# Kernel optimization log

Hardware: AMD Instinct MI355X
Metric: run time of the kernel (lower is better)

Reference implementation:

```python
import jax, jax.numpy as jnp
import numpy as np

H = 1024; NH = 16; HD = H // NH  # hidden, heads, head_dim

def setup_inputs() -> dict:
    key = jax.random.key(0)
    ks = jax.random.split(key, 9)
    s = 1.0 / np.sqrt(H)
    return {
        "hidden_states": jax.random.normal(ks[0], (2, 2048, H), jnp.float32),
        "Wq": jax.random.uniform(ks[1], (H, H), jnp.float32, -s, s),
        "bq": jnp.zeros((H,), jnp.float32),
        "Wk": jax.random.uniform(ks[2], (H, H), jnp.float32, -s, s),
        "bk": jnp.zeros((H,), jnp.float32),
        "Wv": jax.random.uniform(ks[3], (H, H), jnp.float32, -s, s),
        "bv": jnp.zeros((H,), jnp.float32),
        "Wo": jax.random.uniform(ks[4], (H, H), jnp.float32, -s, s),
        "bo": jnp.zeros((H,), jnp.float32),
    }

def reference(hidden_states, Wq, bq, Wk, bk, Wv, bv, Wo, bo):
    B, S, _ = hidden_states.shape
    def heads(x):  # [B,S,H] -> [B,NH,S,HD]
        return x.reshape(B, S, NH, HD).transpose(0, 2, 1, 3)
    q = heads(hidden_states @ Wq + bq)
    k = heads(hidden_states @ Wk + bk)
    v = heads(hidden_states @ Wv + bv)
    scores = jnp.einsum('bhqd,bhkd->bhqk', q, k) / jnp.sqrt(jnp.float32(HD))
    causal = jnp.where(jnp.tril(jnp.ones((S, S), bool)), 0.0, -jnp.inf)
    probs = jax.nn.softmax(scores + causal[None, None], axis=-1)
    ctx = jnp.einsum('bhqk,bhkd->bhqd', probs, v)
    ctx = ctx.transpose(0, 2, 1, 3).reshape(B, S, H)
    return ctx @ Wo + bo
```

## Files before the change

kernel.cpp:

```cpp
#include <hip/hip_runtime.h>
#include <hip/hip_bf16.h>

#define BB 2
#define SS 2048
#define HH 1024
#define NHH 16
#define HDD 64
#define MM (BB*SS)
#define QKV_N (3*HH)

typedef _Float16 f16x8 __attribute__((ext_vector_type(8)));
typedef _Float16 f16x4 __attribute__((ext_vector_type(4)));
typedef float f32x4 __attribute__((ext_vector_type(4)));

#define MFMA16(a,b,c)  __builtin_amdgcn_mfma_f32_16x16x32_f16((a),(b),(c),0,0,0)
#define MFMA16K16(a,b,c) __builtin_amdgcn_mfma_f32_16x16x16f16((a),(b),(c),0,0,0)

__device__ __forceinline__ void gl2lds16(const _Float16* g, _Float16* l) {
    __builtin_amdgcn_global_load_lds(
        (const __attribute__((address_space(1))) void*)g,
        (__attribute__((address_space(3))) void*)l, 16, 0, 0);
}

__device__ __forceinline__ float fexp2(float x) { return __builtin_amdgcn_exp2f(x); }

__global__ __launch_bounds__(256) void prep_kernel(
    const float* __restrict__ X,
    const float* __restrict__ W0, const float* __restrict__ W1,
    const float* __restrict__ W2, const float* __restrict__ W3,
    _Float16* __restrict__ Xh,
    _Float16* __restrict__ WqkvT, _Float16* __restrict__ WoT)
{
    __shared__ float t[64][65];
    int z = blockIdx.z;
    int tid = threadIdx.x;
    if (z == 4) {
        int base = (blockIdx.y * 16 + blockIdx.x) * 256 + tid;
        const float4* xin = (const float4*)X;
        f16x4* xout = (f16x4*)Xh;
#pragma unroll
        for (int i = 0; i < 16; ++i) {
            float4 v = xin[base + i * 65536];
            f16x4 hh = {(_Float16)v.x, (_Float16)v.y, (_Float16)v.z, (_Float16)v.w};
            xout[base + i * 65536] = hh;
        }
        return;
    }
    const float* src = (z == 0) ? W0 : (z == 1) ? W1 : (z == 2) ? W2 : W3;
    _Float16* dst = (z < 3) ? (WqkvT + (size_t)z * HH * HH) : WoT;
    int k0 = blockIdx.y * 64, n0 = blockIdx.x * 64;
#pragma unroll
    for (int p = 0; p < 4; ++p) {
        int row = p * 16 + (tid >> 4);
        int col4 = (tid & 15) * 4;
        float4 v = *(const float4*)&src[(size_t)(k0 + row) * HH + n0 + col4];
        t[row][col4 + 0] = v.x; t[row][col4 + 1] = v.y;
        t[row][col4 + 2] = v.z; t[row][col4 + 3] = v.w;
    }
    __syncthreads();
#pragma unroll
    for (int p = 0; p < 2; ++p) {
        int nc = p * 32 + (tid >> 3);
        int ch = tid & 7;
        f16x8 o;
#pragma unroll
        for (int j = 0; j < 8; ++j) o[j] = (_Float16)t[ch * 8 + j][nc];
        *(f16x8*)&dst[(size_t)(n0 + nc) * HH + k0 + ch * 8] = o;
    }
}

__global__ __launch_bounds__(256, 5) void gemm_qkv_kernel(
    const _Float16* __restrict__ A, const _Float16* __restrict__ Bt,
    const float* __restrict__ bias0, const float* __restrict__ bias1, const float* __restrict__ bias2,
    _Float16* __restrict__ Qh, _Float16* __restrict__ Kh, _Float16* __restrict__ Vt)
{
    const int K = HH;
    const int NT = K / 32;
    __shared__ _Float16 smem[16384];

    int row0 = blockIdx.y * 128, n0 = blockIdx.x * 128;
    int tid = threadIdx.x;
    int w = tid >> 6, l = tid & 63, m16 = l & 15, quad = l >> 4;
    int wm = w >> 1, wn = w & 1;

    int srow = w * 32 + (l >> 2);
    int sch = (l & 3) ^ ((l >> 2) & 3) ^ ((l >> 4) & 3);
    const _Float16* aptr = A + (size_t)(row0 + srow) * K + sch * 8;
    const _Float16* bptr = Bt + (size_t)(n0 + srow) * K + sch * 8;

    int gsw = (m16 & 3) ^ ((m16 >> 2) & 3);
    int acol = (quad ^ gsw) * 8;

    f32x4 zero4 = {0.f, 0.f, 0.f, 0.f};
    f32x4 acc[4][4];
#pragma unroll
    for (int i = 0; i < 4; ++i)
#pragma unroll
        for (int j = 0; j < 4; ++j) acc[i][j] = zero4;

    auto stage = [&](int t) {
        int s = (t & 1) * 4096;
        int k0 = t * 32;
        int ao = s + (w * 32) * 32;
        int bo = 8192 + s + (w * 32) * 32;
        gl2lds16(aptr + k0, smem + ao);
        gl2lds16(aptr + (size_t)16 * K + k0, smem + ao + 16 * 32);
        gl2lds16(bptr + k0, smem + bo);
        gl2lds16(bptr + (size_t)16 * K + k0, smem + bo + 16 * 32);
    };

    stage(0);
    for (int t = 0; t < NT; ++t) {
        asm volatile("s_barrier" ::: "memory");
        if (t + 1 < NT) {
            stage(t + 1);
            asm volatile("s_waitcnt vmcnt(4)" ::: "memory");
        } else {
            asm volatile("s_waitcnt vmcnt(0)" ::: "memory");
        }
        asm volatile("s_barrier" ::: "memory");

        const _Float16* Asr = smem + (t & 1) * 4096;
        const _Float16* Bsr = smem + 8192 + (t & 1) * 4096;
        f16x8 af[4], bf[4];
#pragma unroll
        for (int i = 0; i < 4; ++i)
            af[i] = *(const f16x8*)&Asr[(wm * 64 + i * 16 + m16) * 32 + acol];
#pragma unroll
        for (int j = 0; j < 4; ++j)
            bf[j] = *(const f16x8*)&Bsr[(wn * 64 + j * 16 + m16) * 32 + acol];
#pragma unroll
        for (int i = 0; i < 4; ++i)
#pragma unroll
            for (int j = 0; j < 4; ++j)
                acc[i][j] = MFMA16(af[i], bf[j], acc[i][j]);
    }

    int which = n0 >> 10;
    const float* bias = (which == 0) ? bias0 : (which == 1) ? bias1 : bias2;
    int b = row0 >> 11, s0 = row0 & 2047;

#pragma unroll
    for (int rh = 0; rh < 2; ++rh) {
        __syncthreads();
        if (wm == rh) {
#pragma unroll
            for (int j = 0; j < 4; ++j) {
                int n_local = wn * 64 + j * 16 + m16;
                float bi = bias[(n0 + n_local) & 1023];
#pragma unroll
                for (int i = 0; i < 4; ++i)
#pragma unroll
                    for (int r = 0; r < 4; ++r) {
                        int m_loc = i * 16 + quad * 4 + r;
                        float v = acc[i][j][r] + bi;
                        if (which == 0) v *= 0.18033688011112042f;
                        if (which == 2) smem[n_local * 68 + m_loc] = (_Float16)v;
                        else            smem[m_loc * 132 + n_local] = (_Float16)v;
                    }
            }
        }
        __syncthreads();
        int hs0 = s0 + rh * 64;
        if (which == 2) {
#pragma unroll
            for (int p = 0; p < 4; ++p) {
                int n_local = p * 32 + (tid >> 3);
                int schunk = tid & 7;
                f16x8 v = *(const f16x8*)&smem[n_local * 68 + schunk * 8];
                int nw = (n0 + n_local) & 1023;
                int hh = nw >> 6, d = nw & 63;
                *(f16x8*)&Vt[((size_t)(b * NHH + hh) * HDD + d) * SS + hs0 + schunk * 8] = v;
            }
        } else {
            _Float16* dst = (which == 0) ? Qh : Kh;
            int hh0 = (n0 & 1023) >> 6;
#pragma unroll
            for (int p = 0; p < 4; ++p) {
                int m_local = p * 16 + (tid >> 4);
                int seg = tid & 15;
                f16x8 v = *(const f16x8*)&smem[m_local * 132 + seg * 8];
                int hh = hh0 + (seg >> 3), d = (seg & 7) * 8;
                *(f16x8*)&dst[((size_t)(b * NHH + hh) * SS + hs0 + m_local) * HDD + d] = v;
            }
        }
    }
}

__global__ __launch_bounds__(256) void gemm_out_kernel(
    const _Float16* __restrict__ A, const _Float16* __restrict__ Bt,
    const float* __restrict__ bias0, float* __restrict__ Out)
{
    const int K = HH;
    const int NT = K / 32;
    __shared__ _Float16 smem[24576];

    int row0 = blockIdx.y * 128, n0 = blockIdx.x * 128;
    int tid = threadIdx.x;
    int w = tid >> 6, l = tid & 63, m16 = l & 15, quad = l >> 4;
    int wm = w >> 1, wn = w & 1;

    int srow = w * 32 + (l >> 2);
    int sch = (l & 3) ^ ((l >> 2) & 3) ^ ((l >> 4) & 3);
    const _Float16* aptr = A + (size_t)(row0 + srow) * K + sch * 8;
    const _Float16* bptr = Bt + (size_t)(n0 + srow) * K + sch * 8;

    int gsw = (m16 & 3) ^ ((m16 >> 2) & 3);
    int acol = (quad ^ gsw) * 8;

    f32x4 zero4 = {0.f, 0.f, 0.f, 0.f};
    f32x4 acc[4][4];
#pragma unroll
    for (int i = 0; i < 4; ++i)
#pragma unroll
        for (int j = 0; j < 4; ++j) acc[i][j] = zero4;

    auto stage = [&](int t, int s) {
        int k0 = t * 32;
        int ao = s * 4096 + (w * 32) * 32;
        int bo = 12288 + s * 4096 + (w * 32) * 32;
        gl2lds16(aptr + k0, smem + ao);
        gl2lds16(aptr + (size_t)16 * K + k0, smem + ao + 16 * 32);
        gl2lds16(bptr + k0, smem + bo);
        gl2lds16(bptr + (size_t)16 * K + k0, smem + bo + 16 * 32);
    };

    stage(0, 0);
    stage(1, 1);
    int cur = 0;
    for (int t = 0; t < NT; ++t) {
        if (t < NT - 1) asm volatile("s_waitcnt vmcnt(4)" ::: "memory");
        else            asm volatile("s_waitcnt vmcnt(0)" ::: "memory");
        asm volatile("s_barrier" ::: "memory");
        if (t + 2 < NT) {
            int nxt = cur + 2; if (nxt >= 3) nxt -= 3;
            stage(t + 2, nxt);
        }
        const _Float16* Asr = smem + cur * 4096;
        const _Float16* Bsr = smem + 12288 + cur * 4096;
        f16x8 af[4], bf[4];
#pragma unroll
        for (int i = 0; i < 4; ++i)
            af[i] = *(const f16x8*)&Asr[(wm * 64 + i * 16 + m16) * 32 + acol];
#pragma unroll
        for (int j = 0; j < 4; ++j)
            bf[j] = *(const f16x8*)&Bsr[(wn * 64 + j * 16 + m16) * 32 + acol];
#pragma unroll
        for (int i = 0; i < 4; ++i)
#pragma unroll
            for (int j = 0; j < 4; ++j)
                acc[i][j] = MFMA16(af[i], bf[j], acc[i][j]);
        cur = (cur == 2) ? 0 : cur + 1;
    }

#pragma unroll
    for (int j = 0; j < 4; ++j) {
        int n = n0 + wn * 64 + j * 16 + m16;
        float bi = bias0[n];
#pragma unroll
        for (int i = 0; i < 4; ++i)
#pragma unroll
            for (int r = 0; r < 4; ++r) {
                int mg = row0 + wm * 64 + i * 16 + quad * 4 + r;
                Out[(size_t)mg * HH + n] = acc[i][j][r] + bi;
            }
    }
}

__global__ __launch_bounds__(512, 4) void attn_kernel(
    const _Float16* __restrict__ Qh, const _Float16* __restrict__ Kh,
    const _Float16* __restrict__ Vt, _Float16* __restrict__ Ctx)
{
    __shared__ _Float16 KV[3 * 8192];

    int tid = threadIdx.x;
    int w = tid >> 6, l = tid & 63;
    int m16 = l & 15, quad = l >> 4;
    int b = blockIdx.z, h = blockIdx.y;
    int tA = blockIdx.x, tB = 31 - tA;
    int half = w >> 2, wq = w & 3;
    int myT = half ? tB : tA;

    const _Float16* Q = Qh + (size_t)(b * NHH + h) * SS * HDD;
    const _Float16* K = Kh + (size_t)(b * NHH + h) * SS * HDD;
    const _Float16* V = Vt + (size_t)(b * NHH + h) * HDD * SS;

    int q = myT * 64 + wq * 16 + m16;
    f16x8 aq0 = *(const f16x8*)(Q + (size_t)q * HDD + quad * 8);
    f16x8 aq1 = *(const f16x8*)(Q + (size_t)q * HDD + 32 + quad * 8);

    int srow = w * 8 + (l >> 3);
    int sch = (l & 7) ^ (l >> 3);
    const _Float16* kg = K + (size_t)srow * HDD + sch * 8;
    const _Float16* vg = V + (size_t)srow * SS + sch * 8;

    auto stage = [&](int t, int s) {
        int kt = t * 64;
        _Float16* kb = &KV[s * 8192];
        _Float16* vb = &KV[s * 8192 + 4096];
        gl2lds16(kg + (size_t)kt * HDD, kb + (w * 8) * 64);
        gl2lds16(vg + kt, vb + (w * 8) * 64);
    };

    int swz = m16 & 7;
    int cka = (quad ^ swz) * 8;
    int ckb = ((quad + 4) ^ swz) * 8;
    int vco[4];
#pragma unroll
    for (int s = 0; s < 4; ++s)
        vco[s] = (((s * 2 + (quad >> 1)) ^ swz) * 8) + (quad & 1) * 4;

    f32x4 zero4 = {0.f, 0.f, 0.f, 0.f};
    const f16x4 ones4 = {(_Float16)1.f, (_Float16)1.f, (_Float16)1.f, (_Float16)1.f};
    f32x4 o[4];
#pragma unroll
    for (int c = 0; c < 4; ++c) o[c] = zero4;
    f32x4 lacc = zero4;

    stage(0, 0);
    stage(1, 1);
    int cur = 0;
    for (int t = 0; t <= tB; ++t) {
        int kt = t * 64;
        if (t < tB) asm volatile("s_waitcnt vmcnt(2)" ::: "memory");
        else        asm volatile("s_waitcnt vmcnt(0)" ::: "memory");
        asm volatile("s_barrier" ::: "memory");
        if (t + 2 <= tB) {
            int nxt = cur + 2; if (nxt >= 3) nxt -= 3;
            stage(t + 2, nxt);
        }

        if (t <= myT) {
            const _Float16* kb = &KV[cur * 8192];
            const _Float16* vb = &KV[cur * 8192 + 4096];
            f16x8 bk[4][2];
#pragma unroll
            for (int s = 0; s < 4; ++s) {
                const _Float16* kr = kb + (s * 16 + m16) * 64;
                bk[s][0] = *(const f16x8*)(kr + cka);
                bk[s][1] = *(const f16x8*)(kr + ckb);
            }
            f16x4 av[4][4];
#pragma unroll
            for (int c = 0; c < 4; ++c) {
                const _Float16* vr = vb + (c * 16 + m16) * 64;
#pragma unroll
                for (int s = 0; s < 4; ++s)
                    av[c][s] = *(const f16x4*)(vr + vco[s]);
            }

            f32x4 st[4];
#pragma unroll
            for (int s = 0; s < 4; ++s) {
                st[s] = MFMA16(bk[s][0], aq0, zero4);
                st[s] = MFMA16(bk[s][1], aq1, st[s]);
            }
            f16x4 pt[4];
            if (t == myT) {
#pragma unroll
                for (int s = 0; s < 4; ++s)
#pragma unroll
                    for (int r = 0; r < 4; ++r) {
                        float p = fexp2(st[s][r]);
                        int key = kt + s * 16 + quad * 4 + r;
                        if (key > q) p = 0.f;
                        pt[s][r] = (_Float16)p;
                    }
            } else {
#pragma unroll
                for (int s = 0; s < 4; ++s)
#pragma unroll
                    for (int r = 0; r < 4; ++r)
                        pt[s][r] = (_Float16)fexp2(st[s][r]);
            }
#pragma unroll
            for (int s = 0; s < 4; ++s)
                lacc = MFMA16K16(ones4, pt[s], lacc);
#pragma unroll
            for (int c = 0; c < 4; ++c)
#pragma unroll
                for (int s = 0; s < 4; ++s)
                    o[c] = MFMA16K16(av[c][s], pt[s], o[c]);
        }

        cur = (cur == 2) ? 0 : cur + 1;
    }

    float inv = 1.0f / lacc[0];
    size_t rowoff = ((size_t)(b * SS) + q) * HH + h * HDD;
#pragma unroll
    for (int c = 0; c < 4; ++c) {
        f16x4 ov;
#pragma unroll
        for (int r = 0; r < 4; ++r) ov[r] = (_Float16)(o[c][r] * inv);
        *(f16x4*)&Ctx[rowoff + c * 16 + quad * 4] = ov;
    }
}

extern "C" void kernel_launch(void* const* d_in, const int* in_sizes, int n_in,
                              void* d_out, int out_size, void* d_ws, size_t ws_size,
                              hipStream_t stream) {
    const float* hs = (const float*)d_in[0];
    const float* Wq = (const float*)d_in[1];
    const float* bq = (const float*)d_in[2];
    const float* Wk = (const float*)d_in[3];
    const float* bk = (const float*)d_in[4];
    const float* Wv = (const float*)d_in[5];
    const float* bv = (const float*)d_in[6];
    const float* Wo = (const float*)d_in[7];
    const float* bo = (const float*)d_in[8];
    float* out = (float*)d_out;

    size_t off = 0;
    auto alloc = [&](size_t bytes) {
        void* p = (char*)d_ws + off;
        off += (bytes + 255) & ~(size_t)255;
        return p;
    };
    _Float16* Xh    = (_Float16*)alloc((size_t)MM * HH * 2);
    _Float16* WqkvT = (_Float16*)alloc((size_t)3 * HH * HH * 2);
    _Float16* WoT   = (_Float16*)alloc((size_t)HH * HH * 2);
    _Float16* Qh    = (_Float16*)alloc((size_t)BB * NHH * SS * HDD * 2);
    _Float16* Kh    = (_Float16*)alloc((size_t)BB * NHH * SS * HDD * 2);
    _Float16* Vt    = (_Float16*)alloc((size_t)BB * NHH * SS * HDD * 2);
    _Float16* Ctx   = (_Float16*)alloc((size_t)MM * HH * 2);

    prep_kernel<<<dim3(16, 16, 5), 256, 0, stream>>>(
        hs, Wq, Wk, Wv, Wo, Xh, WqkvT, WoT);
    gemm_qkv_kernel<<<dim3(QKV_N / 128, MM / 128), 256, 0, stream>>>(
        Xh, WqkvT, bq, bk, bv, Qh, Kh, Vt);
    attn_kernel<<<dim3(16, NHH, BB), 512, 0, stream>>>(Qh, Kh, Vt, Ctx);
    gemm_out_kernel<<<dim3(HH / 128, MM / 128), 256, 0, stream>>>(
        Ctx, WoT, bo, out);
}
```

Before: 181.3 us.

## Enlarge QKV GEMM tile to 256x256 with 8 waves and quadrant-interleaved prefetch

```diff
diff --git a/kernel.cpp b/kernel.cpp
--- a/kernel.cpp
+++ b/kernel.cpp
@@ -69,71 +69,130 @@
     }
 }
 
-__global__ __launch_bounds__(256, 5) void gemm_qkv_kernel(
+__global__ __launch_bounds__(512, 2) void gemm_qkv_kernel(
     const _Float16* __restrict__ A, const _Float16* __restrict__ Bt,
     const float* __restrict__ bias0, const float* __restrict__ bias1, const float* __restrict__ bias2,
     _Float16* __restrict__ Qh, _Float16* __restrict__ Kh, _Float16* __restrict__ Vt)
 {
-    const int K = HH;
-    const int NT = K / 32;
-    __shared__ _Float16 smem[16384];
-
-    int row0 = blockIdx.y * 128, n0 = blockIdx.x * 128;
+    __shared__ _Float16 smem[65536];
+
+    int bid = blockIdx.y * 12 + blockIdx.x;
+    int swzb = (bid & 7) * 24 + (bid >> 3);
+    int bx = swzb % 12, by = swzb / 12;
+    int row0 = by * 256, n0 = bx * 256;
+
     int tid = threadIdx.x;
     int w = tid >> 6, l = tid & 63, m16 = l & 15, quad = l >> 4;
-    int wm = w >> 1, wn = w & 1;
-
-    int srow = w * 32 + (l >> 2);
+    int wm = w >> 2, wn = w & 3;
+
+    int srow = w * 16 + (l >> 2);
     int sch = (l & 3) ^ ((l >> 2) & 3) ^ ((l >> 4) & 3);
-    const _Float16* aptr = A + (size_t)(row0 + srow) * K + sch * 8;
-    const _Float16* bptr = Bt + (size_t)(n0 + srow) * K + sch * 8;
+    const _Float16* aptr = A + (size_t)(row0 + srow) * HH + sch * 8;
+    const _Float16* bptr = Bt + (size_t)(n0 + srow) * HH + sch * 8;
 
     int gsw = (m16 & 3) ^ ((m16 >> 2) & 3);
     int acol = (quad ^ gsw) * 8;
 
     f32x4 zero4 = {0.f, 0.f, 0.f, 0.f};
-    f32x4 acc[4][4];
-#pragma unroll
-    for (int i = 0; i < 4; ++i)
+    f32x4 acc[8][4];
+#pragma unroll
+    for (int i = 0; i < 8; ++i)
 #pragma unroll
         for (int j = 0; j < 4; ++j) acc[i][j] = zero4;
 
-    auto stage = [&](int t) {
-        int s = (t & 1) * 4096;
-        int k0 = t * 32;
-        int ao = s + (w * 32) * 32;
-        int bo = 8192 + s + (w * 32) * 32;
-        gl2lds16(aptr + k0, smem + ao);
-        gl2lds16(aptr + (size_t)16 * K + k0, smem + ao + 16 * 32);
-        gl2lds16(bptr + k0, smem + bo);
-        gl2lds16(bptr + (size_t)16 * K + k0, smem + bo + 16 * 32);
+    auto stageA = [&](int s, int h, int ks) {
+        gl2lds16(aptr + (size_t)h * 128 * HH + s * 64 + ks * 32,
+                 smem + (s & 1) * 16384 + ks * 8192 + (h * 128 + w * 16) * 32);
     };
-
-    stage(0);
-    for (int t = 0; t < NT; ++t) {
-        asm volatile("s_barrier" ::: "memory");
-        if (t + 1 < NT) {
-            stage(t + 1);
-            asm volatile("s_waitcnt vmcnt(4)" ::: "memory");
-        } else {
-            asm volatile("s_waitcnt vmcnt(0)" ::: "memory");
-        }
-        asm volatile("s_barrier" ::: "memory");
-
-        const _Float16* Asr = smem + (t & 1) * 4096;
-        const _Float16* Bsr = smem + 8192 + (t & 1) * 4096;
-        f16x8 af[4], bf[4];
-#pragma unroll
-        for (int i = 0; i < 4; ++i)
-            af[i] = *(const f16x8*)&Asr[(wm * 64 + i * 16 + m16) * 32 + acol];
-#pragma unroll
-        for (int j = 0; j < 4; ++j)
-            bf[j] = *(const f16x8*)&Bsr[(wn * 64 + j * 16 + m16) * 32 + acol];
-#pragma unroll
-        for (int i = 0; i < 4; ++i)
-#pragma unroll
-            for (int j = 0; j < 4; ++j)
-                acc[i][j] = MFMA16(af[i], bf[j], acc[i][j]);
+    auto stageB = [&](int s, int h, int ks) {
+        gl2lds16(bptr + (size_t)h * 128 * HH + s * 64 + ks * 32,
+                 smem + 32768 + (s & 1) * 16384 + ks * 8192 + (h * 128 + w * 16) * 32);
+    };
+
+    stageA(0, 0, 0); stageA(0, 0, 1); stageA(0, 1, 0); stageA(0, 1, 1);
+    stageB(0, 0, 0); stageB(0, 0, 1); stageB(0, 1, 0); stageB(0, 1, 1);
+
+    for (int s = 0; s < 16; ++s) {
+        const _Float16* Ab = smem + (s & 1) * 16384;
+        const _Float16* Bb = smem + 32768 + (s & 1) * 16384;
+        bool pf = (s + 1 < 16);
+        f16x8 af[4][2], bf[2][2];
+
+        if (pf) { stageA(s + 1, 0, 0); stageA(s + 1, 0, 1);
+                  asm volatile("s_waitcnt vmcnt(2)" ::: "memory"); }
+        else    { asm volatile("s_waitcnt vmcnt(0)" ::: "memory"); }
+        asm volatile("s_barrier" ::: "memory");
+#pragma unroll
+        for (int fi = 0; fi < 4; ++fi)
+#pragma unroll
+            for (int ks = 0; ks < 2; ++ks)
+                af[fi][ks] = *(const f16x8*)&Ab[ks * 8192 + (wm * 128 + fi * 16 + m16) * 32 + acol];
+#pragma unroll
+        for (int fj = 0; fj < 2; ++fj)
+#pragma unroll
+            for (int ks = 0; ks < 2; ++ks)
+                bf[fj][ks] = *(const f16x8*)&Bb[ks * 8192 + (wn * 64 + fj * 16 + m16) * 32 + acol];
+        __builtin_amdgcn_s_setprio(1);
+#pragma unroll
+        for (int fi = 0; fi < 4; ++fi)
+#pragma unroll
+            for (int fj = 0; fj < 2; ++fj) {
+                acc[fi][fj] = MFMA16(af[fi][0], bf[fj][0], acc[fi][fj]);
+                acc[fi][fj] = MFMA16(af[fi][1], bf[fj][1], acc[fi][fj]);
+            }
+        __builtin_amdgcn_s_setprio(0);
+        asm volatile("s_barrier" ::: "memory");
+
+        if (pf) { stageA(s + 1, 1, 0); stageA(s + 1, 1, 1); }
+#pragma unroll
+        for (int fj = 0; fj < 2; ++fj)
+#pragma unroll
+            for (int ks = 0; ks < 2; ++ks)
+                bf[fj][ks] = *(const f16x8*)&Bb[ks * 8192 + (wn * 64 + 32 + fj * 16 + m16) * 32 + acol];
+        __builtin_amdgcn_s_setprio(1);
+#pragma unroll
+        for (int fi = 0; fi < 4; ++fi)
+#pragma unroll
+            for (int fj = 0; fj < 2; ++fj) {
+                acc[fi][2 + fj] = MFMA16(af[fi][0], bf[fj][0], acc[fi][2 + fj]);
+                acc[fi][2 + fj] = MFMA16(af[fi][1], bf[fj][1], acc[fi][2 + fj]);
+            }
+        __builtin_amdgcn_s_setprio(0);
+        asm volatile("s_barrier" ::: "memory");
+
+        if (pf) { stageB(s + 1, 0, 0); stageB(s + 1, 0, 1); }
+#pragma unroll
+        for (int fi = 0; fi < 4; ++fi)
+#pragma unroll
+            for (int ks = 0; ks < 2; ++ks)
+                af[fi][ks] = *(const f16x8*)&Ab[ks * 8192 + (wm * 128 + 64 + fi * 16 + m16) * 32 + acol];
+        __builtin_amdgcn_s_setprio(1);
+#pragma unroll
+        for (int fi = 0; fi < 4; ++fi)
+#pragma unroll
+            for (int fj = 0; fj < 2; ++fj) {
+                acc[4 + fi][2 + fj] = MFMA16(af[fi][0], bf[fj][0], acc[4 + fi][2 + fj]);
+                acc[4 + fi][2 + fj] = MFMA16(af[fi][1], bf[fj][1], acc[4 + fi][2 + fj]);
+            }
+        __builtin_amdgcn_s_setprio(0);
+        asm volatile("s_barrier" ::: "memory");
+
+        if (pf) { stageB(s + 1, 1, 0); stageB(s + 1, 1, 1); }
+#pragma unroll
+        for (int fj = 0; fj < 2; ++fj)
+#pragma unroll
+            for (int ks = 0; ks < 2; ++ks)
+                bf[fj][ks] = *(const f16x8*)&Bb[ks * 8192 + (wn * 64 + fj * 16 + m16) * 32 + acol];
+        __builtin_amdgcn_s_setprio(1);
+#pragma unroll
+        for (int fi = 0; fi < 4; ++fi)
+#pragma unroll
+            for (int fj = 0; fj < 2; ++fj) {
+                acc[4 + fi][fj] = MFMA16(af[fi][0], bf[fj][0], acc[4 + fi][fj]);
+                acc[4 + fi][fj] = MFMA16(af[fi][1], bf[fj][1], acc[4 + fi][fj]);
+            }
+        __builtin_amdgcn_s_setprio(0);
+        asm volatile("s_barrier" ::: "memory");
     }
 
     int which = n0 >> 10;
@@ -149,25 +208,25 @@
                 int n_local = wn * 64 + j * 16 + m16;
                 float bi = bias[(n0 + n_local) & 1023];
 #pragma unroll
-                for (int i = 0; i < 4; ++i)
+                for (int i = 0; i < 8; ++i)
 #pragma unroll
                     for (int r = 0; r < 4; ++r) {
                         int m_loc = i * 16 + quad * 4 + r;
                         float v = acc[i][j][r] + bi;
                         if (which == 0) v *= 0.18033688011112042f;
-                        if (which == 2) smem[n_local * 68 + m_loc] = (_Float16)v;
-                        else            smem[m_loc * 132 + n_local] = (_Float16)v;
+                        if (which == 2) smem[n_local * 136 + m_loc] = (_Float16)v;
+                        else            smem[m_loc * 264 + n_local] = (_Float16)v;
                     }
             }
         }
         __syncthreads();
-        int hs0 = s0 + rh * 64;
+        int hs0 = s0 + rh * 128;
         if (which == 2) {
 #pragma unroll
-            for (int p = 0; p < 4; ++p) {
-                int n_local = p * 32 + (tid >> 3);
-                int schunk = tid & 7;
-                f16x8 v = *(const f16x8*)&smem[n_local * 68 + schunk * 8];
+            for (int p = 0; p < 8; ++p) {
+                int n_local = p * 32 + (tid >> 4);
+                int schunk = tid & 15;
+                f16x8 v = *(const f16x8*)&smem[n_local * 136 + schunk * 8];
                 int nw = (n0 + n_local) & 1023;
                 int hh = nw >> 6, d = nw & 63;
                 *(f16x8*)&Vt[((size_t)(b * NHH + hh) * HDD + d) * SS + hs0 + schunk * 8] = v;
@@ -176,10 +235,10 @@
             _Float16* dst = (which == 0) ? Qh : Kh;
             int hh0 = (n0 & 1023) >> 6;
 #pragma unroll
-            for (int p = 0; p < 4; ++p) {
-                int m_local = p * 16 + (tid >> 4);
-                int seg = tid & 15;
-                f16x8 v = *(const f16x8*)&smem[m_local * 132 + seg * 8];
+            for (int p = 0; p < 8; ++p) {
+                int m_local = p * 16 + (tid >> 5);
+                int seg = tid & 31;
+                f16x8 v = *(const f16x8*)&smem[m_local * 264 + seg * 8];
                 int hh = hh0 + (seg >> 3), d = (seg & 7) * 8;
                 *(f16x8*)&dst[((size_t)(b * NHH + hh) * SS + hs0 + m_local) * HDD + d] = v;
             }
@@ -427,7 +486,7 @@
 
     prep_kernel<<<dim3(16, 16, 5), 256, 0, stream>>>(
         hs, Wq, Wk, Wv, Wo, Xh, WqkvT, WoT);
-    gemm_qkv_kernel<<<dim3(QKV_N / 128, MM / 128), 256, 0, stream>>>(
+    gemm_qkv_kernel<<<dim3(QKV_N / 256, MM / 256), 512, 0, stream>>>(
         Xh, WqkvT, bq, bk, bv, Qh, Kh, Vt);
     attn_kernel<<<dim3(16, NHH, BB), 512, 0, stream>>>(Qh, Kh, Vt, Ctx);
     gemm_out_kernel<<<dim3(HH / 128, MM / 128), 256, 0, stream>>>(
```

New measurement: 185.2 us. 1.02x slower.
